# Optimization experiments

Hardware: AMD Instinct MI355X
Metric: run time of the kernel (lower is better)

The kernel has to match this reference:

```python
import jax, jax.numpy as jnp
import numpy as np

B, S, D = 2, 2048, 1024
H = 16
HD = D // H  # 64


def setup_inputs() -> dict:
    key = jax.random.key(0)
    ks = jax.random.split(key, 6)
    x = jax.random.normal(ks[0], (B, S, D), dtype=jnp.float32)
    sc = 1.0 / np.sqrt(D)
    Wq = jax.random.normal(ks[1], (D, D), dtype=jnp.float32) * sc
    Wk = jax.random.normal(ks[2], (D, D), dtype=jnp.float32) * sc
    Wv = jax.random.normal(ks[3], (D, D), dtype=jnp.float32) * sc
    Wo = jax.random.normal(ks[4], (D, D), dtype=jnp.float32) * sc
    bo = jax.random.normal(ks[5], (D,), dtype=jnp.float32) * 0.01
    return {"x": x, "Wq": Wq, "Wk": Wk, "Wv": Wv, "Wo": Wo, "bo": bo}


def reference(x, Wq, Wk, Wv, Wo, bo):
    b, s, d = x.shape
    # projections (torch Linear: y = x @ W.T; weights here stored as [d_in, d_out])
    Q = (x @ Wq).reshape(b, s, H, HD).transpose(0, 2, 1, 3)  # [b,h,s,hd]
    K = (x @ Wk).reshape(b, s, H, HD).transpose(0, 2, 1, 3)
    V = (x @ Wv).reshape(b, s, H, HD).transpose(0, 2, 1, 3)
    scores = jnp.einsum("bhqd,bhkd->bhqk", Q, K) / np.sqrt(HD)
    causal = jnp.triu(jnp.ones((s, s), dtype=bool), k=1)  # True above diagonal
    scores = jnp.where(causal[None, None], -jnp.inf, scores)
    attn = jax.nn.softmax(scores, axis=-1)
    # dropout_rate = 0.0 -> identity (eval-mode reference)
    ctx = jnp.einsum("bhqk,bhkd->bhqd", attn, V)
    ctx = ctx.transpose(0, 2, 1, 3).reshape(b, s, d)
    return ctx @ Wo + bo
```

## Files before the change

kernel.cpp:

```cpp
#include <hip/hip_runtime.h>
#include <hip/hip_bf16.h>

#define B_  2
#define S_  2048
#define D_  1024
#define H_  16
#define HD_ 64
#define M_  (B_*S_)

typedef __attribute__((ext_vector_type(8))) short short8;
typedef __attribute__((ext_vector_type(4))) float f32x4;

#define MFMA16(a, b, c) __builtin_amdgcn_mfma_f32_16x16x32_bf16((a), (b), (c), 0, 0, 0)

static __device__ inline short f2bf(float f) {
    union { float f; unsigned u; } v; v.f = f;
    unsigned r = v.u + 0x7FFFu + ((v.u >> 16) & 1u);
    return (short)(r >> 16);
}

static __device__ __forceinline__ float fexp2(float x) {
    float r;
    asm volatile("v_exp_f32 %0, %1\n\ts_nop 1" : "=v"(r) : "v"(x));
    return r;
}

static __device__ __forceinline__ unsigned cvt_pk_bf16(float lo, float hi) {
    unsigned r;
    asm volatile("v_cvt_pk_bf16_f32 %0, %1, %2" : "=v"(r) : "v"(lo), "v"(hi));
    return r;
}

static __device__ __forceinline__ void gl_lds16(const short* g, short* l) {
    __builtin_amdgcn_global_load_lds(
        (const __attribute__((address_space(1))) void*)g,
        (__attribute__((address_space(3))) void*)l, 16, 0, 0);
}

__global__ void cvt_x_kernel(const float* __restrict__ x, short* __restrict__ xb, int n4) {
    int i = blockIdx.x * blockDim.x + threadIdx.x;
    int stride = gridDim.x * blockDim.x;
    for (; i < n4; i += stride) {
        float4 v = ((const float4*)x)[i];
        short4 o;
        o.x = f2bf(v.x); o.y = f2bf(v.y); o.z = f2bf(v.z); o.w = f2bf(v.w);
        ((short4*)xb)[i] = o;
    }
}

__global__ void transpose_w_kernel(const float* __restrict__ W, short* __restrict__ Wt) {
    __shared__ float tile[32][33];
    int tx = threadIdx.x & 31, ty = threadIdx.x >> 5;
    int n0 = blockIdx.x * 32, k0 = blockIdx.y * 32;
#pragma unroll
    for (int i = 0; i < 4; ++i)
        tile[ty + 8 * i][tx] = W[(size_t)(k0 + ty + 8 * i) * D_ + n0 + tx];
    __syncthreads();
#pragma unroll
    for (int i = 0; i < 4; ++i)
        Wt[(size_t)(n0 + ty + 8 * i) * D_ + k0 + tx] = f2bf(tile[tx][ty + 8 * i]);
}

template <int MODE>
__global__ __launch_bounds__(256) void gemm128(const short* __restrict__ A,
                                               const short* __restrict__ Bt,
                                               const float* __restrict__ bias,
                                               void* __restrict__ out, int NB) {
    __shared__ __align__(16) short Asm[128 * 32];
    __shared__ __align__(16) short Bsm[128 * 32];
    int bm = blockIdx.x / NB, bn = blockIdx.x % NB;
    int tid = threadIdx.x, l = tid & 63, w = tid >> 6;
    int lhi = l >> 4, llo = l & 15;
    int wm = w >> 1, wn = w & 1;

    f32x4 acc[4][4];
#pragma unroll
    for (int m = 0; m < 4; ++m)
#pragma unroll
        for (int n = 0; n < 4; ++n) acc[m][n] = (f32x4){0.f, 0.f, 0.f, 0.f};

    const short* Ag = A + (size_t)(bm * 128) * 1024;
    const short* Bg = Bt + (size_t)(bn * 128) * 1024;
    int c0 = tid, c1 = 256 + tid;
    int r0 = ((c0 >> 5) << 3) | (c0 & 7), s0 = ((c0 >> 3) & 3) ^ (r0 & 3);
    int r1 = ((c1 >> 5) << 3) | (c1 & 7), s1 = ((c1 >> 3) & 3) ^ (r1 & 3);

    for (int k0 = 0; k0 < 1024; k0 += 32) {
        gl_lds16(Ag + (size_t)r0 * 1024 + k0 + s0 * 8, &Asm[c0 * 8]);
        gl_lds16(Ag + (size_t)r1 * 1024 + k0 + s1 * 8, &Asm[c1 * 8]);
        gl_lds16(Bg + (size_t)r0 * 1024 + k0 + s0 * 8, &Bsm[c0 * 8]);
        gl_lds16(Bg + (size_t)r1 * 1024 + k0 + s1 * 8, &Bsm[c1 * 8]);
        __syncthreads();
        short8 af[4], bf[4];
#pragma unroll
        for (int m = 0; m < 4; ++m) {
            int row = wm * 64 + m * 16 + llo;
            int ci = ((row >> 3) << 5) | (((lhi ^ row) & 3) << 3) | (row & 7);
            af[m] = *(const short8*)&Asm[ci * 8];
        }
#pragma unroll
        for (int n = 0; n < 4; ++n) {
            int row = wn * 64 + n * 16 + llo;
            int ci = ((row >> 3) << 5) | (((lhi ^ row) & 3) << 3) | (row & 7);
            bf[n] = *(const short8*)&Bsm[ci * 8];
        }
#pragma unroll
        for (int m = 0; m < 4; ++m)
#pragma unroll
            for (int n = 0; n < 4; ++n)
                acc[m][n] = MFMA16(af[m], bf[n], acc[m][n]);
        __syncthreads();
    }

    int rowb = bm * 128 + wm * 64, colb = bn * 128 + wn * 64;
#pragma unroll
    for (int m = 0; m < 4; ++m) {
#pragma unroll
        for (int n = 0; n < 4; ++n) {
            int col = colb + n * 16 + llo;
#pragma unroll
            for (int j = 0; j < 4; ++j) {
                int row = rowb + m * 16 + lhi * 4 + j;
                float v = acc[m][n][j];
                if (MODE == 2) {
                    ((float*)out)[(size_t)row * 1024 + col] = v + bias[col];
                } else {
                    int proj = col >> 10, n1 = col & 1023;
                    int h = n1 >> 6, hd = n1 & 63;
                    int b = row >> 11, s = row & 2047;
                    short* o = (short*)out;
                    size_t off;
                    if (proj == 0)
                        off = ((size_t)(b * 16 + h) * 2048 + s) * 64 + hd;
                    else if (proj == 1)
                        off = (size_t)M_ * D_ + ((size_t)(b * 16 + h) * 2048 + s) * 64 + hd;
                    else
                        off = (size_t)2 * M_ * D_ + ((size_t)(b * 16 + h) * 64 + hd) * 2048 + s;
                    o[off] = f2bf(v);
                }
            }
        }
    }
}

__global__ __launch_bounds__(512) void attn_kernel(const short* __restrict__ Q,
                                                   const short* __restrict__ Kg,
                                                   const short* __restrict__ Vt,
                                                   short* __restrict__ ctx) {
    __shared__ __align__(16) char kvbuf[2][16384];
    __shared__ __align__(16) char plds[8][2048];
    int tid = threadIdx.x, w = tid >> 6, l = tid & 63;
    int lhi = l >> 4, llo = l & 15;
    int bh = blockIdx.x & 31, qp = blockIdx.x >> 5;
    int b = bh >> 4, h = bh & 15;
    char* pb = plds[w];

    const short* Qh = Q + (size_t)bh * S_ * HD_;
    const short* Kh = Kg + (size_t)bh * S_ * HD_;
    const short* Vh = Vt + (size_t)bh * HD_ * S_;

    int qbA = qp, qbB = 15 - qp;
    int NTA = 2 * qp + 2;
    const int NT = 34;

    int srow = tid >> 3;
    int ssrc = (16 * (tid & 7)) ^ ((srow & 7) << 4);
    auto stage = [&](char* buf, int c0) {
        gl_lds16(Kh + (size_t)(c0 + srow) * HD_ + (ssrc >> 1), (short*)(buf + tid * 16));
        gl_lds16(Vh + (size_t)srow * S_ + c0 + (ssrc >> 1), (short*)(buf + 8192 + tid * 16));
    };

    f32x4 O[4];
#pragma unroll
    for (int n = 0; n < 4; ++n) O[n] = (f32x4){0.f, 0.f, 0.f, 0.f};
    float lpart[4] = {0.f, 0.f, 0.f, 0.f};

    auto writeOut = [&](int qb) {
        int qbs = qb * 128 + w * 16;
#pragma unroll
        for (int j = 0; j < 4; ++j) {
            float ls = lpart[j];
            ls += __shfl_xor(ls, 1);
            ls += __shfl_xor(ls, 2);
            ls += __shfl_xor(ls, 4);
            ls += __shfl_xor(ls, 8);
            float inv = 1.0f / ls;
            int row = qbs + lhi * 4 + j;
            size_t base = ((size_t)(b * S_ + row)) * D_ + h * HD_;
#pragma unroll
            for (int n = 0; n < 4; ++n)
                ctx[base + n * 16 + llo] = f2bf(O[n][j] * inv);
        }
    };

    const float SC = 0.18033688f;
    const float M2 = 17.312340f;

    int qbase = qbA * 128 + w * 16;
    short8 aq0 = *(const short8*)(Qh + (size_t)(qbase + llo) * HD_ + 8 * lhi);
    short8 aq1 = *(const short8*)(Qh + (size_t)(qbase + llo) * HD_ + 32 + 8 * lhi);

    stage(kvbuf[0], 0);

    for (int i = 0; i < NT; ++i) {
        asm volatile("s_waitcnt vmcnt(0)" ::: "memory");
        __builtin_amdgcn_s_barrier();
        asm volatile("" ::: "memory");
        int kt = (i < NTA) ? i : i - NTA;
        int c0 = kt * 64;
        if (i + 1 < NT) {
            int ni = i + 1;
            int nkt = (ni < NTA) ? ni : ni - NTA;
            stage(kvbuf[ni & 1], nkt * 64);
        }
        const char* kb = kvbuf[i & 1];
        const char* vb = kb + 8192;

        if (c0 <= qbase + 15) {
            f32x4 sc4[4];
#pragma unroll
            for (int cb = 0; cb < 4; ++cb) {
                int row = cb * 16 + llo;
                int sw = (row & 7) << 4;
                short8 kf0 = *(const short8*)(kb + row * 128 + ((16 * lhi) ^ sw));
                short8 kf1 = *(const short8*)(kb + row * 128 + ((64 + 16 * lhi) ^ sw));
                f32x4 z = (f32x4){0.f, 0.f, 0.f, 0.f};
                z = MFMA16(aq0, kf0, z);
                z = MFMA16(aq1, kf1, z);
                sc4[cb] = z;
            }
            bool diag = (c0 + 63 > qbase);
#pragma unroll
            for (int j = 0; j < 4; ++j) {
                int qr = qbase + lhi * 4 + j;
                float v0 = fmaf(sc4[0][j], SC, -M2);
                float v1 = fmaf(sc4[1][j], SC, -M2);
                float v2 = fmaf(sc4[2][j], SC, -M2);
                float v3 = fmaf(sc4[3][j], SC, -M2);
                if (diag) {
                    if (c0 + llo > qr)      v0 = -1e30f;
                    if (c0 + 16 + llo > qr) v1 = -1e30f;
                    if (c0 + 32 + llo > qr) v2 = -1e30f;
                    if (c0 + 48 + llo > qr) v3 = -1e30f;
                }
                float p0 = fexp2(v0), p1 = fexp2(v1);
                float p2 = fexp2(v2), p3 = fexp2(v3);
                lpart[j] += (p0 + p1) + (p2 + p3);
                unsigned pk01 = cvt_pk_bf16(p0, p1);
                unsigned pk23 = cvt_pk_bf16(p2, p3);
                int r = lhi * 4 + j;
                char* rb = pb + r * 128;
                int sw = (r & 7) << 4;
                *(short*)(rb + ((2 * llo) ^ sw))      = (short)(pk01);
                *(short*)(rb + ((2 * llo + 32) ^ sw)) = (short)(pk01 >> 16);
                *(short*)(rb + ((2 * llo + 64) ^ sw)) = (short)(pk23);
                *(short*)(rb + ((2 * llo + 96) ^ sw)) = (short)(pk23 >> 16);
            }
            int swr = (llo & 7) << 4;
            short8 pa0 = *(const short8*)(pb + llo * 128 + ((16 * lhi) ^ swr));
            short8 pa1 = *(const short8*)(pb + llo * 128 + ((64 + 16 * lhi) ^ swr));
#pragma unroll
            for (int n = 0; n < 4; ++n) {
                int row = n * 16 + llo;
                int sw = (row & 7) << 4;
                short8 vf0 = *(const short8*)(vb + row * 128 + ((16 * lhi) ^ sw));
                short8 vf1 = *(const short8*)(vb + row * 128 + ((64 + 16 * lhi) ^ sw));
                O[n] = MFMA16(pa0, vf0, O[n]);
                O[n] = MFMA16(pa1, vf1, O[n]);
            }
        }

        if (i == NTA - 1) {
            writeOut(qbA);
#pragma unroll
            for (int n = 0; n < 4; ++n) O[n] = (f32x4){0.f, 0.f, 0.f, 0.f};
            lpart[0] = lpart[1] = lpart[2] = lpart[3] = 0.f;
            qbase = qbB * 128 + w * 16;
            aq0 = *(const short8*)(Qh + (size_t)(qbase + llo) * HD_ + 8 * lhi);
            aq1 = *(const short8*)(Qh + (size_t)(qbase + llo) * HD_ + 32 + 8 * lhi);
        }
    }
    writeOut(qbB);
}

extern "C" void kernel_launch(void* const* d_in, const int* in_sizes, int n_in,
                              void* d_out, int out_size, void* d_ws, size_t ws_size,
                              hipStream_t stream) {
    const float* x  = (const float*)d_in[0];
    const float* Wq = (const float*)d_in[1];
    const float* Wk = (const float*)d_in[2];
    const float* Wv = (const float*)d_in[3];
    const float* Wo = (const float*)d_in[4];
    const float* bo = (const float*)d_in[5];
    float* out = (float*)d_out;

    char* ws = (char*)d_ws;
    short* xb    = (short*)(ws);
    short* Wqkvt = (short*)(ws + (size_t)(8 << 20));
    short* Wot   = (short*)(ws + (size_t)(14 << 20));
    short* Qb    = (short*)(ws + (size_t)(16 << 20));
    short* Kb    = Qb + (size_t)M_ * D_;
    short* Vtb   = Qb + (size_t)2 * M_ * D_;
    short* ctx   = xb;

    cvt_x_kernel<<<2048, 256, 0, stream>>>(x, xb, M_ * D_ / 4);
    dim3 tg(32, 32);
    transpose_w_kernel<<<tg, 256, 0, stream>>>(Wq, Wqkvt);
    transpose_w_kernel<<<tg, 256, 0, stream>>>(Wk, Wqkvt + (1 << 20));
    transpose_w_kernel<<<tg, 256, 0, stream>>>(Wv, Wqkvt + (2 << 20));
    transpose_w_kernel<<<tg, 256, 0, stream>>>(Wo, Wot);

    gemm128<0><<<32 * 24, 256, 0, stream>>>(xb, Wqkvt, nullptr, Qb, 24);
    attn_kernel<<<256, 512, 0, stream>>>(Qb, Kb, Vtb, ctx);
    gemm128<2><<<32 * 8, 256, 0, stream>>>(ctx, Wot, bo, out, 8);
}
```

Before: 150.5 us.

## Double-buffer GEMM LDS tiles and remap block indices across XCDs

The projection GEMM now keeps two LDS buffers and issues the next K-slice's global-to-LDS loads right after a barrier, so the loads can overlap with the current slice's MFMAs. This replaces the two barriers per iteration with one. The LDS fragment offsets are hoisted out of the loop, and block IDs are remapped so that each of 8 chiplet groups handles a contiguous range of N-tiles, which should improve L2 reuse. The cost is twice the LDS use per block, which may lower occupancy. The remap also assumes NB is divisible by 8.

```diff
diff --git a/kernel.cpp b/kernel.cpp
--- a/kernel.cpp
+++ b/kernel.cpp
@@ -66,9 +66,11 @@
                                                const short* __restrict__ Bt,
                                                const float* __restrict__ bias,
                                                void* __restrict__ out, int NB) {
-    __shared__ __align__(16) short Asm[128 * 32];
-    __shared__ __align__(16) short Bsm[128 * 32];
-    int bm = blockIdx.x / NB, bn = blockIdx.x % NB;
+    __shared__ __align__(16) short Asm[2][128 * 32];
+    __shared__ __align__(16) short Bsm[2][128 * 32];
+    int NBX = NB >> 3;
+    int X = blockIdx.x & 7, t = blockIdx.x >> 3;
+    int bm = t / NBX, bn = X * NBX + t % NBX;
     int tid = threadIdx.x, l = tid & 63, w = tid >> 6;
     int lhi = l >> 4, llo = l & 15;
     int wm = w >> 1, wn = w & 1;
@@ -85,31 +87,42 @@
     int r0 = ((c0 >> 5) << 3) | (c0 & 7), s0 = ((c0 >> 3) & 3) ^ (r0 & 3);
     int r1 = ((c1 >> 5) << 3) | (c1 & 7), s1 = ((c1 >> 3) & 3) ^ (r1 & 3);
 
-    for (int k0 = 0; k0 < 1024; k0 += 32) {
-        gl_lds16(Ag + (size_t)r0 * 1024 + k0 + s0 * 8, &Asm[c0 * 8]);
-        gl_lds16(Ag + (size_t)r1 * 1024 + k0 + s1 * 8, &Asm[c1 * 8]);
-        gl_lds16(Bg + (size_t)r0 * 1024 + k0 + s0 * 8, &Bsm[c0 * 8]);
-        gl_lds16(Bg + (size_t)r1 * 1024 + k0 + s1 * 8, &Bsm[c1 * 8]);
-        __syncthreads();
+    auto stage = [&](int buf, int k0) {
+        gl_lds16(Ag + (size_t)r0 * 1024 + k0 + s0 * 8, &Asm[buf][c0 * 8]);
+        gl_lds16(Ag + (size_t)r1 * 1024 + k0 + s1 * 8, &Asm[buf][c1 * 8]);
+        gl_lds16(Bg + (size_t)r0 * 1024 + k0 + s0 * 8, &Bsm[buf][c0 * 8]);
+        gl_lds16(Bg + (size_t)r1 * 1024 + k0 + s1 * 8, &Bsm[buf][c1 * 8]);
+    };
+
+    int cia[4], cib[4];
+#pragma unroll
+    for (int m = 0; m < 4; ++m) {
+        int row = wm * 64 + m * 16 + llo;
+        cia[m] = ((row >> 3) << 5) | (((lhi ^ row) & 3) << 3) | (row & 7);
+    }
+#pragma unroll
+    for (int n = 0; n < 4; ++n) {
+        int row = wn * 64 + n * 16 + llo;
+        cib[n] = ((row >> 3) << 5) | (((lhi ^ row) & 3) << 3) | (row & 7);
+    }
+
+    stage(0, 0);
+    for (int i = 0; i < 32; ++i) {
+        asm volatile("s_waitcnt vmcnt(0)" ::: "memory");
+        __builtin_amdgcn_s_barrier();
+        asm volatile("" ::: "memory");
+        if (i + 1 < 32) stage((i + 1) & 1, (i + 1) * 32);
+        int cur = i & 1;
         short8 af[4], bf[4];
 #pragma unroll
-        for (int m = 0; m < 4; ++m) {
-            int row = wm * 64 + m * 16 + llo;
-            int ci = ((row >> 3) << 5) | (((lhi ^ row) & 3) << 3) | (row & 7);
-            af[m] = *(const short8*)&Asm[ci * 8];
-        }
-#pragma unroll
-        for (int n = 0; n < 4; ++n) {
-            int row = wn * 64 + n * 16 + llo;
-            int ci = ((row >> 3) << 5) | (((lhi ^ row) & 3) << 3) | (row & 7);
-            bf[n] = *(const short8*)&Bsm[ci * 8];
-        }
+        for (int m = 0; m < 4; ++m) af[m] = *(const short8*)&Asm[cur][cia[m] * 8];
+#pragma unroll
+        for (int n = 0; n < 4; ++n) bf[n] = *(const short8*)&Bsm[cur][cib[n] * 8];
 #pragma unroll
         for (int m = 0; m < 4; ++m)
 #pragma unroll
             for (int n = 0; n < 4; ++n)
                 acc[m][n] = MFMA16(af[m], bf[n], acc[m][n]);
-        __syncthreads();
     }
 
     int rowb = bm * 128 + wm * 64, colb = bn * 128 + wn * 64;
```

New measurement: 146.6 us. 1.03x faster.
